# Performance work log

Hardware: AMD Instinct MI355X
Metric: run time of the kernel (lower is better)

## Reference

```python
import jax, jax.numpy as jnp
import numpy as np

N = 50000
EPS = 1e-5


def gcn_conv(x, W, b, src, dst, n):
    # x: [n, Cin]; W: [Cin, Cout]; src/dst: [E+n] with self-loops included
    h = x @ W  # dense GEMM
    deg = jax.ops.segment_sum(jnp.ones_like(dst, dtype=h.dtype), dst, num_segments=n)
    dinv = jnp.where(deg > 0, jax.lax.rsqrt(deg), 0.0)
    norm = dinv[src] * dinv[dst]  # [E+n]
    msgs = h[src] * norm[:, None]  # gather + scale
    out = jax.ops.segment_sum(msgs, dst, num_segments=n)  # scatter-add
    return out + b


def batch_norm(x, gamma, beta, mean, var):
    return (x - mean) * jax.lax.rsqrt(var + EPS) * gamma + beta


def setup_inputs() -> dict:
    key = jax.random.key(0)
    ks = jax.random.split(key, 16)
    IN, H, OUT, E = 1280, 256, 500, 1600000
    x = jax.random.normal(ks[0], (N, IN), dtype=jnp.float32)
    edge_index = jax.random.randint(ks[1], (2, E), 0, N, dtype=jnp.int64)
    def lin(k, cin, cout):
        return jax.random.normal(k, (cin, cout), dtype=jnp.float32) / np.sqrt(cin)
    return {
        "x": x,
        "edge_index": edge_index,
        "W1": lin(ks[2], IN, H), "b1": jnp.zeros((H,), jnp.float32),
        "g1": jnp.ones((H,), jnp.float32), "be1": jnp.zeros((H,), jnp.float32),
        "m1": 0.1 * jax.random.normal(ks[3], (H,), jnp.float32),
        "v1": 0.5 + jax.random.uniform(ks[4], (H,), jnp.float32),
        "W2": lin(ks[5], H, H), "b2": jnp.zeros((H,), jnp.float32),
        "g2": jnp.ones((H,), jnp.float32), "be2": jnp.zeros((H,), jnp.float32),
        "m2": 0.1 * jax.random.normal(ks[6], (H,), jnp.float32),
        "v2": 0.5 + jax.random.uniform(ks[7], (H,), jnp.float32),
        "W3": lin(ks[8], H, OUT), "b3": jnp.zeros((OUT,), jnp.float32),
    }


def reference(x, edge_index, W1, b1, g1, be1, m1, v1, W2, b2, g2, be2, m2, v2, W3, b3):
    n = x.shape[0]
    loops = jnp.arange(n, dtype=edge_index.dtype)
    src = jnp.concatenate([edge_index[0], loops])
    dst = jnp.concatenate([edge_index[1], loops])
    h = gcn_conv(x, W1, b1, src, dst, n)
    h = jax.nn.relu(batch_norm(h, g1, be1, m1, v1))
    h = gcn_conv(h, W2, b2, src, dst, n)
    h = jax.nn.relu(batch_norm(h, g2, be2, m2, v2))
    return gcn_conv(h, W3, b3, src, dst, n)
```

## Files before the change

### kernel.cpp

```cpp
#include <hip/hip_runtime.h>
#include <hip/hip_bf16.h>
#include <stdint.h>

typedef __attribute__((ext_vector_type(4))) float f32x4;
typedef __attribute__((ext_vector_type(8))) short s16x8;
typedef __attribute__((ext_vector_type(4))) unsigned short u16x4;

#define EPSBN 1e-5f

__device__ __forceinline__ float bf2f(unsigned short u) {
  union { unsigned int i; float f; } w; w.i = ((unsigned int)u) << 16; return w.f;
}
__device__ __forceinline__ unsigned short f2bf(float f) {
  __hip_bfloat16 h = __float2bfloat16(f);
  unsigned short u; __builtin_memcpy(&u, &h, 2); return u;
}
__device__ __forceinline__ void gld_lds16(const void* g, void* l) {
  __builtin_amdgcn_global_load_lds(
      (const __attribute__((address_space(1))) void*)(g),
      (__attribute__((address_space(3))) void*)(l), 16, 0, 0);
}

__global__ void k_init_deg(unsigned* deg, int n) {
  int i = blockIdx.x * 256 + threadIdx.x;
  if (i < n) deg[i] = 1u;
}
__global__ void k_count(const int* __restrict__ dst, unsigned* __restrict__ deg, int E) {
  int i = blockIdx.x * 256 + threadIdx.x;
  if (i < E) atomicAdd(&deg[dst[i]], 1u);
}
__global__ void k_dinv(const unsigned* __restrict__ deg, float* __restrict__ dinv, int n) {
  int i = blockIdx.x * 256 + threadIdx.x;
  if (i < n) dinv[i] = rsqrtf((float)deg[i]);
}
__global__ void k_bsum(const unsigned* __restrict__ deg, unsigned* __restrict__ bsum, int n) {
  __shared__ unsigned s[256];
  int t = threadIdx.x, i = blockIdx.x * 256 + t;
  s[t] = (i < n) ? deg[i] : 0u;
  __syncthreads();
  for (int st = 128; st > 0; st >>= 1) {
    if (t < st) s[t] += s[t + st];
    __syncthreads();
  }
  if (t == 0) bsum[blockIdx.x] = s[0];
}
__global__ void k_scan_top(const unsigned* __restrict__ bsum, unsigned* __restrict__ bpre,
                           int nb, unsigned* __restrict__ offs, int n) {
  __shared__ unsigned s[256];
  int t = threadIdx.x;
  unsigned v = (t < nb) ? bsum[t] : 0u;
  s[t] = v; __syncthreads();
  for (int d = 1; d < 256; d <<= 1) {
    unsigned a = (t >= d) ? s[t - d] : 0u;
    __syncthreads();
    s[t] += a;
    __syncthreads();
  }
  bpre[t] = s[t] - v;
  if (t == 255) offs[n] = s[255];
}
__global__ void k_scan_fin(const unsigned* __restrict__ deg, const unsigned* __restrict__ bpre,
                           unsigned* __restrict__ offs, unsigned* __restrict__ cur, int n) {
  __shared__ unsigned s[256];
  int t = threadIdx.x, i = blockIdx.x * 256 + t;
  unsigned v = (i < n) ? deg[i] : 0u;
  s[t] = v; __syncthreads();
  for (int d = 1; d < 256; d <<= 1) {
    unsigned a = (t >= d) ? s[t - d] : 0u;
    __syncthreads();
    s[t] += a;
    __syncthreads();
  }
  if (i < n) {
    unsigned o = bpre[blockIdx.x] + s[t] - v;
    offs[i] = o; cur[i] = o;
  }
}
__global__ void k_fill(const int* __restrict__ src, const int* __restrict__ dst,
                       unsigned* __restrict__ cur, int* __restrict__ adj, int E, int n) {
  int i = blockIdx.x * 256 + threadIdx.x;
  int s, d;
  if (i < E)          { s = src[i]; d = dst[i]; }
  else if (i < E + n) { s = d = i - E; }
  else return;
  unsigned p = atomicAdd(&cur[d], 1u);
  adj[p] = s;
}
__global__ __launch_bounds__(256) void k_sortw(const unsigned* __restrict__ offs,
                                               const int* __restrict__ adj,
                                               const float* __restrict__ dinv,
                                               int2* __restrict__ ew, int nN) {
  int wv = (blockIdx.x * 256 + threadIdx.x) >> 6;
  int lane = threadIdx.x & 63;
  if (wv >= nN) return;
  unsigned beg = offs[wv], end = offs[wv + 1];
  int len = (int)(end - beg);
  float dv = dinv[wv];
  if (len <= 64) {
    int k = (lane < len) ? adj[beg + lane] : 0x7FFFFFFF;
#pragma unroll
    for (int size = 2; size <= 64; size <<= 1) {
#pragma unroll
      for (int stride = size >> 1; stride > 0; stride >>= 1) {
        int other = __shfl_xor(k, stride);
        bool up = (lane & size) == 0;
        bool lower = (lane & stride) == 0;
        k = (lower == up) ? min(k, other) : max(k, other);
      }
    }
    if (lane < len) ew[beg + lane] = make_int2(k, __float_as_int(dinv[k] * dv));
  } else {
    for (unsigned e = beg + lane; e < end; e += 64) {
      int s = adj[e];
      ew[e] = make_int2(s, __float_as_int(dinv[s] * dv));
    }
  }
}
__global__ void k_wt(const float* __restrict__ W, unsigned short* __restrict__ Wt,
                     int K, int N, int Npad) {
  int idx = blockIdx.x * 256 + threadIdx.x;
  if (idx >= Npad * K) return;
  int nn = idx / K, k = idx - nn * K;
  float v = (nn < N) ? W[(size_t)k * N + nn] : 0.f;
  Wt[idx] = f2bf(v);
}

#define BM 128
#define BN 128
#define BK 64

template<int OUTF32>
__global__ __launch_bounds__(256, 4) void k_gemm(
    const unsigned short* __restrict__ Au, const unsigned short* __restrict__ Bt,
    void* __restrict__ Coutv, const float* __restrict__ bias,
    int M, int N, int K, int MT, int NT)
{
  __shared__ __align__(16) unsigned short As[BM * BK];
  __shared__ __align__(16) unsigned short Bs[BN * BK];

  int d = blockIdx.x;
  int xc = d & 7, sb = d >> 3;
  int nt = sb % NT, mt = (sb / NT) * 8 + xc;
  if (mt >= MT) return;
  int m0 = mt * BM, n0 = nt * BN;

  int tid = threadIdx.x, lane = tid & 63, wave = tid >> 6;
  int wm = wave >> 1, wn = wave & 1;
  int l15 = lane & 15, l4 = lane >> 4;

  f32x4 acc[4][4];
#pragma unroll
  for (int i = 0; i < 4; ++i)
#pragma unroll
    for (int j = 0; j < 4; ++j) acc[i][j] = 0.f;

  int srow[4], scg[4];
#pragma unroll
  for (int i = 0; i < 4; ++i) {
    int ci = (wave + 4 * i) * 64 + lane;
    srow[i] = ci >> 3;
    scg[i] = (ci & 7) ^ (srow[i] & 7);
  }

  int nk = K / BK;
  for (int kt = 0; kt < nk; ++kt) {
    __syncthreads();
#pragma unroll
    for (int i = 0; i < 4; ++i) {
      int gr = m0 + srow[i]; gr = gr < M ? gr : M - 1;
      gld_lds16(Au + (size_t)gr * K + kt * BK + scg[i] * 8, As + (wave + 4 * i) * 512);
    }
#pragma unroll
    for (int i = 0; i < 4; ++i) {
      int gn = n0 + srow[i];
      gld_lds16(Bt + (size_t)gn * K + kt * BK + scg[i] * 8, Bs + (wave + 4 * i) * 512);
    }
    __syncthreads();

#pragma unroll
    for (int ks = 0; ks < 2; ++ks) {
      s16x8 af[4], bf[4];
#pragma unroll
      for (int f = 0; f < 4; ++f) {
        int r = wm * 64 + f * 16 + l15;
        int ca = (ks * 4 + l4) ^ (r & 7);
        af[f] = *(const s16x8*)(As + r * 64 + ca * 8);
        int nloc = wn * 64 + f * 16 + l15;
        int cb = (ks * 4 + l4) ^ (nloc & 7);
        bf[f] = *(const s16x8*)(Bs + nloc * 64 + cb * 8);
      }
#pragma unroll
      for (int fm = 0; fm < 4; ++fm)
#pragma unroll
        for (int fn = 0; fn < 4; ++fn)
          acc[fm][fn] = __builtin_amdgcn_mfma_f32_16x16x32_bf16(af[fm], bf[fn], acc[fm][fn], 0, 0, 0);
    }
  }

#pragma unroll
  for (int fm = 0; fm < 4; ++fm) {
#pragma unroll
    for (int fn = 0; fn < 4; ++fn) {
#pragma unroll
      for (int r = 0; r < 4; ++r) {
        int row = m0 + wm * 64 + fm * 16 + l4 * 4 + r;
        int col = n0 + wn * 64 + fn * 16 + l15;
        if (row < M && col < N) {
          if (OUTF32)
            ((float*)Coutv)[(size_t)row * N + col] = acc[fm][fn][r] + bias[col];
          else
            ((unsigned short*)Coutv)[(size_t)row * N + col] = f2bf(acc[fm][fn][r]);
        }
      }
    }
  }
}

__global__ __launch_bounds__(256, 3) void k_gemmF(
    const float* __restrict__ Af, const unsigned short* __restrict__ Bt,
    unsigned short* __restrict__ Cout, int M, int N, int K, int MT, int NT)
{
  __shared__ __align__(16) float As[BM * BK];
  __shared__ __align__(16) unsigned short Bs[BN * BK];

  int d = blockIdx.x;
  int xc = d & 7, sb = d >> 3;
  int nt = sb % NT, mt = (sb / NT) * 8 + xc;
  if (mt >= MT) return;
  int m0 = mt * BM, n0 = nt * BN;

  int tid = threadIdx.x, lane = tid & 63, wave = tid >> 6;
  int wm = wave >> 1, wn = wave & 1;
  int l15 = lane & 15, l4 = lane >> 4;

  f32x4 acc[4][4];
#pragma unroll
  for (int i = 0; i < 4; ++i)
#pragma unroll
    for (int j = 0; j < 4; ++j) acc[i][j] = 0.f;

  int arow[8], acs[8];
#pragma unroll
  for (int i = 0; i < 8; ++i) {
    int ci = (i * 4 + wave) * 64 + lane;
    arow[i] = ci >> 4;
    acs[i] = (ci & 15) ^ ((arow[i] & 7) << 1);
  }
  int brow[4], bcg[4];
#pragma unroll
  for (int i = 0; i < 4; ++i) {
    int ci = (i * 4 + wave) * 64 + lane;
    brow[i] = ci >> 3;
    bcg[i] = (ci & 7) ^ (brow[i] & 7);
  }

  int nk = K / BK;
  for (int kt = 0; kt < nk; ++kt) {
    __syncthreads();
#pragma unroll
    for (int i = 0; i < 8; ++i) {
      int gr = m0 + arow[i]; gr = gr < M ? gr : M - 1;
      gld_lds16(Af + (size_t)gr * K + kt * BK + acs[i] * 4, As + (i * 4 + wave) * 256);
    }
#pragma unroll
    for (int i = 0; i < 4; ++i) {
      int gn = n0 + brow[i];
      gld_lds16(Bt + (size_t)gn * K + kt * BK + bcg[i] * 8, Bs + (i * 4 + wave) * 512);
    }
    __syncthreads();

#pragma unroll
    for (int ks = 0; ks < 2; ++ks) {
      s16x8 af[4], bf[4];
#pragma unroll
      for (int f = 0; f < 4; ++f) {
        int r = wm * 64 + f * 16 + l15;
        int c0 = (2 * (ks * 4 + l4)) ^ ((r & 7) << 1);
        f32x4 a0 = *(const f32x4*)(As + r * 64 + c0 * 4);
        f32x4 a1 = *(const f32x4*)(As + r * 64 + c0 * 4 + 4);
        s16x8 pk;
        pk[0] = (short)f2bf(a0[0]); pk[1] = (short)f2bf(a0[1]);
        pk[2] = (short)f2bf(a0[2]); pk[3] = (short)f2bf(a0[3]);
        pk[4] = (short)f2bf(a1[0]); pk[5] = (short)f2bf(a1[1]);
        pk[6] = (short)f2bf(a1[2]); pk[7] = (short)f2bf(a1[3]);
        af[f] = pk;
        int nloc = wn * 64 + f * 16 + l15;
        int cb = (ks * 4 + l4) ^ (nloc & 7);
        bf[f] = *(const s16x8*)(Bs + nloc * 64 + cb * 8);
      }
#pragma unroll
      for (int fm = 0; fm < 4; ++fm)
#pragma unroll
        for (int fn = 0; fn < 4; ++fn)
          acc[fm][fn] = __builtin_amdgcn_mfma_f32_16x16x32_bf16(af[fm], bf[fn], acc[fm][fn], 0, 0, 0);
    }
  }

#pragma unroll
  for (int fm = 0; fm < 4; ++fm) {
#pragma unroll
    for (int fn = 0; fn < 4; ++fn) {
#pragma unroll
      for (int r = 0; r < 4; ++r) {
        int row = m0 + wm * 64 + fm * 16 + l4 * 4 + r;
        int col = n0 + wn * 64 + fn * 16 + l15;
        if (row < M && col < N)
          Cout[(size_t)row * N + col] = f2bf(acc[fm][fn][r]);
      }
    }
  }
}

__device__ __forceinline__ void accum4(float& a0, float& a1, float& a2, float& a3,
                                       u16x4 q, float w) {
  a0 += bf2f(q[0]) * w; a1 += bf2f(q[1]) * w;
  a2 += bf2f(q[2]) * w; a3 += bf2f(q[3]) * w;
}

template<int BNRELU, int BIAS>
__global__ __launch_bounds__(256) void k_agg(
    const unsigned short* __restrict__ h, const int2* __restrict__ ew,
    const unsigned* __restrict__ offs, const float* __restrict__ bias,
    const float* __restrict__ gam, const float* __restrict__ bet,
    const float* __restrict__ mea, const float* __restrict__ var,
    unsigned short* __restrict__ outp, int nN)
{
  const int C = 256;
  int wave = threadIdx.x >> 6, lane = threadIdx.x & 63;
  int v = blockIdx.x * 4 + wave;
  if (v >= nN) return;
  unsigned beg = offs[v], end = offs[v + 1];
  int len = (int)(end - beg);
  int ch0 = lane * 4;
  const unsigned short* hb = h + ch0;
  float a0 = 0, a1 = 0, a2 = 0, a3 = 0;

  for (int base = 0; base < len; base += 64) {
    int m = min(64, len - base);
    int2 myp = make_int2(0, 0);
    if (lane < m) myp = ew[beg + base + lane];
    int ng = (m + 7) >> 3;

    u16x4 q[8]; float w[8];
#pragma unroll
    for (int r = 0; r < 8; ++r) {
      int s = __shfl(myp.x, r);
      w[r] = __int_as_float(__shfl(myp.y, r));
      q[r] = *(const u16x4*)(hb + (size_t)s * C);
    }
    for (int g = 1; g < ng; ++g) {
      u16x4 q2[8]; float w2[8];
#pragma unroll
      for (int r = 0; r < 8; ++r) {
        int b = g * 8 + r;
        int s = __shfl(myp.x, b);
        w2[r] = __int_as_float(__shfl(myp.y, b));
        q2[r] = *(const u16x4*)(hb + (size_t)s * C);
      }
#pragma unroll
      for (int r = 0; r < 8; ++r) accum4(a0, a1, a2, a3, q[r], w[r]);
#pragma unroll
      for (int r = 0; r < 8; ++r) { q[r] = q2[r]; w[r] = w2[r]; }
    }
#pragma unroll
    for (int r = 0; r < 8; ++r) accum4(a0, a1, a2, a3, q[r], w[r]);
  }

  float va[4] = {a0, a1, a2, a3};
#pragma unroll
  for (int j = 0; j < 4; ++j) {
    int ch = ch0 + j;
    float val = va[j];
    if (BIAS) val += bias[ch];
    if (BNRELU) {
      val = (val - mea[ch]) * rsqrtf(var[ch] + EPSBN) * gam[ch] + bet[ch];
      val = fmaxf(val, 0.f);
    }
    outp[(size_t)v * C + ch] = f2bf(val);
  }
}

extern "C" void kernel_launch(void* const* d_in, const int* in_sizes, int n_in,
                              void* d_out, int out_size, void* d_ws, size_t ws_size,
                              hipStream_t stream) {
  const float* x   = (const float*)d_in[0];
  const int*   ei  = (const int*)d_in[1];
  const float* W1  = (const float*)d_in[2];
  const float* b1  = (const float*)d_in[3];
  const float* g1  = (const float*)d_in[4];
  const float* be1 = (const float*)d_in[5];
  const float* m1  = (const float*)d_in[6];
  const float* v1  = (const float*)d_in[7];
  const float* W2  = (const float*)d_in[8];
  const float* b2  = (const float*)d_in[9];
  const float* g2  = (const float*)d_in[10];
  const float* be2 = (const float*)d_in[11];
  const float* m2  = (const float*)d_in[12];
  const float* v2  = (const float*)d_in[13];
  const float* W3  = (const float*)d_in[14];
  const float* b3  = (const float*)d_in[15];

  const int IN = 1280, H = 256, OUT = 500, OUTP = 512;
  int E  = in_sizes[1] / 2;
  int nN = in_sizes[0] / IN;
  const int* srcI = ei;
  const int* dstI = ei + E;

  char* p = (char*)d_ws;
  auto carve = [&](size_t bytes) { char* r = p; p += (bytes + 511) & ~(size_t)511; return r; };
  unsigned short* Wt1 = (unsigned short*)carve((size_t)H * IN * 2);
  unsigned short* Wt2 = (unsigned short*)carve((size_t)H * H * 2);
  unsigned short* Wt3 = (unsigned short*)carve((size_t)OUTP * H * 2);
  unsigned* deg  = (unsigned*)carve((size_t)nN * 4);
  float*    dinv = (float*)carve((size_t)nN * 4);
  unsigned* offs = (unsigned*)carve((size_t)(nN + 1) * 4);
  unsigned* cur  = (unsigned*)carve((size_t)nN * 4);
  unsigned* bsum = (unsigned*)carve(256 * 4);
  unsigned* bpre = (unsigned*)carve(256 * 4);
  int*      adj  = (int*)carve((size_t)(E + nN) * 4);
  int2*     ew   = (int2*)carve((size_t)(E + nN) * 8);
  unsigned short* bufA = (unsigned short*)carve((size_t)nN * H * 2);
  unsigned short* bufB = (unsigned short*)carve((size_t)nN * H * 2);

  int NB = (nN + 255) / 256;
  k_init_deg<<<NB, 256, 0, stream>>>(deg, nN);
  k_count<<<(E + 255) / 256, 256, 0, stream>>>(dstI, deg, E);
  k_dinv<<<NB, 256, 0, stream>>>(deg, dinv, nN);
  k_bsum<<<NB, 256, 0, stream>>>(deg, bsum, nN);
  k_scan_top<<<1, 256, 0, stream>>>(bsum, bpre, NB, offs, nN);
  k_scan_fin<<<NB, 256, 0, stream>>>(deg, bpre, offs, cur, nN);
  k_fill<<<(E + nN + 255) / 256, 256, 0, stream>>>(srcI, dstI, cur, adj, E, nN);
  k_sortw<<<(nN + 3) / 4, 256, 0, stream>>>(offs, adj, dinv, ew, nN);

  k_wt<<<(H * IN + 255) / 256, 256, 0, stream>>>(W1, Wt1, IN, H, H);
  k_wt<<<(H * H + 255) / 256, 256, 0, stream>>>(W2, Wt2, H, H, H);
  k_wt<<<(OUTP * H + 255) / 256, 256, 0, stream>>>(W3, Wt3, H, OUT, OUTP);

  int MT = (nN + BM - 1) / BM;
  int mg = (MT + 7) / 8;
  int nAgg = (nN + 3) / 4;

  k_gemmF<<<mg * 8 * 2, 256, 0, stream>>>(x, Wt1, bufA, nN, H, IN, MT, 2);
  k_agg<1, 1><<<nAgg, 256, 0, stream>>>(bufA, ew, offs, b1, g1, be1, m1, v1, bufB, nN);
  k_gemm<0><<<mg * 8 * 2, 256, 0, stream>>>(bufB, Wt2, bufA, nullptr, nN, H, H, MT, 2);
  k_agg<1, 1><<<nAgg, 256, 0, stream>>>(bufA, ew, offs, b2, g2, be2, m2, v2, bufB, nN);
  k_agg<0, 0><<<nAgg, 256, 0, stream>>>(bufB, ew, offs, nullptr, nullptr, nullptr, nullptr, nullptr, bufA, nN);
  k_gemm<1><<<mg * 8 * 4, 256, 0, stream>>>(bufA, Wt3, d_out, b3, nN, OUT, H, MT, 4);
}
```

Before: 701.9 us.

## Fuse prep kernels, merge weight transposes, deepen aggregation gather batches to 16

Merges the dinv and block-sum kernels into one pass over deg, and folds the three weight-transpose launches into a single launch with hardcoded shapes. In the aggregation kernel, the gather batch grows from 8 to 16 rows per group, and edge weights are fetched by shuffle at accumulate time instead of being held in registers. The goal is fewer launches and more memory-level parallelism in the gather. The cost is higher register pressure in the aggregation kernel and weight-transpose code that only works for these fixed sizes.

New measurement: 697.5 us. No clear change (-0.6%).

```diff
diff --git a/kernel.cpp b/kernel.cpp
--- a/kernel.cpp
+++ b/kernel.cpp
@@ -29,14 +29,13 @@
   int i = blockIdx.x * 256 + threadIdx.x;
   if (i < E) atomicAdd(&deg[dst[i]], 1u);
 }
-__global__ void k_dinv(const unsigned* __restrict__ deg, float* __restrict__ dinv, int n) {
-  int i = blockIdx.x * 256 + threadIdx.x;
-  if (i < n) dinv[i] = rsqrtf((float)deg[i]);
-}
-__global__ void k_bsum(const unsigned* __restrict__ deg, unsigned* __restrict__ bsum, int n) {
+__global__ void k_prep2(const unsigned* __restrict__ deg, float* __restrict__ dinv,
+                        unsigned* __restrict__ bsum, int n) {
   __shared__ unsigned s[256];
   int t = threadIdx.x, i = blockIdx.x * 256 + t;
-  s[t] = (i < n) ? deg[i] : 0u;
+  unsigned d = (i < n) ? deg[i] : 0u;
+  if (i < n) dinv[i] = rsqrtf((float)d);
+  s[t] = d;
   __syncthreads();
   for (int st = 128; st > 0; st >>= 1) {
     if (t < st) s[t] += s[t + st];
@@ -116,10 +115,16 @@
     }
   }
 }
-__global__ void k_wt(const float* __restrict__ W, unsigned short* __restrict__ Wt,
-                     int K, int N, int Npad) {
+__global__ void k_wt3(const float* __restrict__ W1, unsigned short* __restrict__ Wt1,
+                      const float* __restrict__ W2, unsigned short* __restrict__ Wt2,
+                      const float* __restrict__ W3, unsigned short* __restrict__ Wt3) {
+  const int n1 = 256 * 1280, n2 = 256 * 256, n3 = 512 * 256;
   int idx = blockIdx.x * 256 + threadIdx.x;
-  if (idx >= Npad * K) return;
+  const float* W; unsigned short* Wt; int K, N;
+  if (idx < n1)            { W = W1; Wt = Wt1; K = 1280; N = 256; }
+  else if (idx < n1 + n2)  { W = W2; Wt = Wt2; K = 256;  N = 256; idx -= n1; }
+  else if (idx < n1+n2+n3) { W = W3; Wt = Wt3; K = 256;  N = 500; idx -= n1 + n2; }
+  else return;
   int nn = idx / K, k = idx - nn * K;
   float v = (nn < N) ? W[(size_t)k * N + nn] : 0.f;
   Wt[idx] = f2bf(v);
@@ -339,31 +344,34 @@
     int m = min(64, len - base);
     int2 myp = make_int2(0, 0);
     if (lane < m) myp = ew[beg + base + lane];
-    int ng = (m + 7) >> 3;
-
-    u16x4 q[8]; float w[8];
-#pragma unroll
-    for (int r = 0; r < 8; ++r) {
+    int ng = (m + 15) >> 4;
+
+    u16x4 q[16];
+#pragma unroll
+    for (int r = 0; r < 16; ++r) {
       int s = __shfl(myp.x, r);
-      w[r] = __int_as_float(__shfl(myp.y, r));
       q[r] = *(const u16x4*)(hb + (size_t)s * C);
     }
     for (int g = 1; g < ng; ++g) {
-      u16x4 q2[8]; float w2[8];
-#pragma unroll
-      for (int r = 0; r < 8; ++r) {
-        int b = g * 8 + r;
-        int s = __shfl(myp.x, b);
-        w2[r] = __int_as_float(__shfl(myp.y, b));
+      u16x4 q2[16];
+#pragma unroll
+      for (int r = 0; r < 16; ++r) {
+        int s = __shfl(myp.x, g * 16 + r);
         q2[r] = *(const u16x4*)(hb + (size_t)s * C);
       }
 #pragma unroll
-      for (int r = 0; r < 8; ++r) accum4(a0, a1, a2, a3, q[r], w[r]);
-#pragma unroll
-      for (int r = 0; r < 8; ++r) { q[r] = q2[r]; w[r] = w2[r]; }
-    }
-#pragma unroll
-    for (int r = 0; r < 8; ++r) accum4(a0, a1, a2, a3, q[r], w[r]);
+      for (int r = 0; r < 16; ++r) {
+        float w = __int_as_float(__shfl(myp.y, (g - 1) * 16 + r));
+        accum4(a0, a1, a2, a3, q[r], w);
+      }
+#pragma unroll
+      for (int r = 0; r < 16; ++r) q[r] = q2[r];
+    }
+#pragma unroll
+    for (int r = 0; r < 16; ++r) {
+      float w = __int_as_float(__shfl(myp.y, (ng - 1) * 16 + r));
+      accum4(a0, a1, a2, a3, q[r], w);
+    }
   }
 
   float va[4] = {a0, a1, a2, a3};
@@ -425,16 +433,12 @@
   int NB = (nN + 255) / 256;
   k_init_deg<<<NB, 256, 0, stream>>>(deg, nN);
   k_count<<<(E + 255) / 256, 256, 0, stream>>>(dstI, deg, E);
-  k_dinv<<<NB, 256, 0, stream>>>(deg, dinv, nN);
-  k_bsum<<<NB, 256, 0, stream>>>(deg, bsum, nN);
+  k_prep2<<<NB, 256, 0, stream>>>(deg, dinv, bsum, nN);
   k_scan_top<<<1, 256, 0, stream>>>(bsum, bpre, NB, offs, nN);
   k_scan_fin<<<NB, 256, 0, stream>>>(deg, bpre, offs, cur, nN);
   k_fill<<<(E + nN + 255) / 256, 256, 0, stream>>>(srcI, dstI, cur, adj, E, nN);
   k_sortw<<<(nN + 3) / 4, 256, 0, stream>>>(offs, adj, dinv, ew, nN);
-
-  k_wt<<<(H * IN + 255) / 256, 256, 0, stream>>>(W1, Wt1, IN, H, H);
-  k_wt<<<(H * H + 255) / 256, 256, 0, stream>>>(W2, Wt2, H, H, H);
-  k_wt<<<(OUTP * H + 255) / 256, 256, 0, stream>>>(W3, Wt3, H, OUT, OUTP);
+  k_wt3<<<(H * IN + H * H + OUTP * H + 255) / 256, 256, 0, stream>>>(W1, Wt1, W2, Wt2, W3, Wt3);
 
   int MT = (nN + BM - 1) / BM;
   int mg = (MT + 7) / 8;
```
